# Optimization experiments

Hardware: AMD Instinct MI355X
Metric: run time of the kernel (lower is better)

Reference implementation:

```python
import jax, jax.numpy as jnp
import numpy as np

D_MODEL = 256
N_HEADS = 8
S_LOCAL = (3, 3)
EPS = 1e-6
B, T, H, W = 2, 4, 32, 32


def _neighbor_idx(Hs, Ws, kh, kw):
    # Replicates nn.Unfold(kernel=(kh,kw), padding=(kh//2,kw//2), stride=1) ordering:
    # kernel offsets row-major, spatial positions row-major.
    off_i = np.repeat(np.arange(kh) - kh // 2, kw)  # (L,)
    off_j = np.tile(np.arange(kw) - kw // 2, kh)    # (L,)
    pi, pj = np.meshgrid(np.arange(Hs), np.arange(Ws), indexing='ij')
    ni = pi.reshape(-1, 1) + off_i[None, :]  # (N, L)
    nj = pj.reshape(-1, 1) + off_j[None, :]
    valid = (ni >= 0) & (ni < Hs) & (nj >= 0) & (nj < Ws)
    idx = np.clip(ni, 0, Hs - 1) * Ws + np.clip(nj, 0, Ws - 1)
    return jnp.asarray(idx, dtype=jnp.int32), jnp.asarray(valid)


def setup_inputs() -> dict:
    key = jax.random.key(0)
    ks = jax.random.split(key, 10)
    D = D_MODEL
    x = jax.random.normal(ks[0], (B, D, T, H, W), dtype=jnp.float32)
    w = lambda k: jax.random.normal(k, (D, D), dtype=jnp.float32) * 0.02
    return {
        'x': x,
        'gamma': jnp.ones((D,), jnp.float32),
        'beta': jnp.zeros((D,), jnp.float32),
        'Wq': w(ks[1]), 'Wk': w(ks[2]), 'Wv': w(ks[3]),
        'Wkl': w(ks[4]), 'Wvl': w(ks[5]), 'Wo': w(ks[6]),
        'q_bias': jax.random.normal(ks[7], (1, N_HEADS, 1, D // N_HEADS), dtype=jnp.float32) * 0.02,
    }


def reference(x, gamma, beta, Wq, Wk, Wv, Wkl, Wvl, Wo, q_bias):
    Bx, D, Tx, Hx, Wx = x.shape
    N = Hx * Wx
    BT = Bx * Tx
    h = N_HEADS
    dh = D // h
    factor = dh ** -0.5

    # (B, D, T, H, W) -> (B*T, H*W, D)
    xr = x.transpose(0, 2, 3, 4, 1).reshape(BT, N, D)
    mu = xr.mean(-1, keepdims=True)
    var = ((xr - mu) ** 2).mean(-1, keepdims=True)
    xn = (xr - mu) * jax.lax.rsqrt(var + EPS) * gamma + beta

    def proj(Wm):
        return (xn @ Wm.T).reshape(BT, N, h, dh).transpose(0, 2, 1, 3)  # (BT, h, N, dh)

    q = proj(Wq) + q_bias
    k = proj(Wk)
    v = proj(Wv)
    kl = proj(Wkl)
    vl = proj(Wvl)

    idx, valid = _neighbor_idx(Hx, Wx, *S_LOCAL)  # (N, L)
    k_nb = kl[:, :, idx, :]  # (BT, h, N, L, dh) -- gather instead of im2col
    v_nb = vl[:, :, idx, :]

    attn_global = jnp.einsum('bhnd,bhgd->bhng', q, k) * factor         # (BT,h,N,N)
    attn_local = jnp.einsum('bhnd,bhnld->bhnl', q, k_nb)               # (BT,h,N,L)
    attn_local = jnp.where(valid[None, None], attn_local, -jnp.inf) * factor

    attn = jax.nn.softmax(jnp.concatenate([attn_global, attn_local], axis=-1), axis=-1)
    a_g, a_l = attn[..., :N], attn[..., N:]

    xg = jnp.einsum('bhng,bhgd->bhnd', a_g, v)
    xl = jnp.einsum('bhnl,bhnld->bhnd', a_l, v_nb)
    out = ((xg + xl).transpose(0, 2, 1, 3).reshape(BT, N, D)) @ Wo.T
    return out.reshape(Bx, Tx, Hx, Wx, D).transpose(0, 4, 1, 2, 3)
```

## Files before the change

kernel.cpp:

```cpp
#include <hip/hip_runtime.h>

#define MCONST 8.0f

typedef float f32x4 __attribute__((ext_vector_type(4)));
typedef __bf16 bf16x8 __attribute__((ext_vector_type(8)));
typedef __bf16 bf16x4 __attribute__((ext_vector_type(4)));


__global__ __launch_bounds__(256) void ln_kernel(const float* __restrict__ x,
                                                 const float* __restrict__ gamma,
                                                 const float* __restrict__ beta,
                                                 __bf16* __restrict__ xfh,
                                                 __bf16* __restrict__ xfl,
                                                 const float* __restrict__ Wq,
                                                 const float* __restrict__ Wk,
                                                 const float* __restrict__ Wv,
                                                 const float* __restrict__ Wkl,
                                                 const float* __restrict__ Wvl,
                                                 const float* __restrict__ Wo,
                                                 __bf16* __restrict__ wh,
                                                 __bf16* __restrict__ wl) {
  __shared__ float red[2][8][32];
  const int blk = blockIdx.x;
  if (blk >= 256) {
    const int gid = (blk - 256) * 256 + threadIdx.x;
    const int mat = gid >> 14;
    const int e = (gid & 16383) * 4;
    const float* W = (mat == 0) ? Wq : (mat == 1) ? Wk : (mat == 2) ? Wv
                     : (mat == 3) ? Wkl : (mat == 4) ? Wvl : Wo;
    const float4 f = *(const float4*)(W + e);
    const int o = e >> 8, k = e & 255;
    const size_t frag = (size_t)mat * 65536 + ((o >> 4) * 8 + (k >> 5)) * 512 +
                        (((k & 31) >> 3) * 16 + (o & 15)) * 8 + (k & 7);
    bf16x4 h, l;
    h[0] = (__bf16)f.x; l[0] = (__bf16)(f.x - (float)h[0]);
    h[1] = (__bf16)f.y; l[1] = (__bf16)(f.y - (float)h[1]);
    h[2] = (__bf16)f.z; l[2] = (__bf16)(f.z - (float)h[2]);
    h[3] = (__bf16)f.w; l[3] = (__bf16)(f.w - (float)h[3]);
    *(bf16x4*)(wh + frag) = h;
    *(bf16x4*)(wl + frag) = l;
    return;
  }
  const int bt = blk >> 5;
  const int b = bt >> 2, t = bt & 3;
  const int n0 = (blk & 31) << 5;
  const int part = threadIdx.x >> 5, r = threadIdx.x & 31;
  const int n = n0 + r;
  const float* xp = x + ((size_t)(b * 256) * 4 + t) * 1024 + n;
  float sum = 0.f, sumsq = 0.f;
#pragma unroll 8
  for (int dd = 0; dd < 32; ++dd) {
    float vv = xp[(size_t)(part * 32 + dd) * 4096];
    sum += vv;
    sumsq += vv * vv;
  }
  red[0][part][r] = sum;
  red[1][part][r] = sumsq;
  __syncthreads();
  float s1 = 0.f, s2 = 0.f;
#pragma unroll
  for (int p = 0; p < 8; ++p) {
    s1 += red[0][p][r];
    s2 += red[1][p][r];
  }
  const float mu = s1 * (1.0f / 256.0f);
  const float var = s2 * (1.0f / 256.0f) - mu * mu;
  const float rstd = rsqrtf(var + 1e-6f);
  const size_t row = (size_t)bt * 1024 + n;
  __bf16 hbuf[32], lbuf[32];
#pragma unroll 8
  for (int dd = 0; dd < 32; ++dd) {
    const int d = part * 32 + dd;
    float vv = xp[(size_t)d * 4096];
    const float val = (vv - mu) * rstd * gamma[d] + beta[d];
    const __bf16 h = (__bf16)val;
    hbuf[dd] = h;
    lbuf[dd] = (__bf16)(val - (float)h);
  }
  const size_t base = ((row >> 4) * 8 + part) * 512 + (row & 15) * 8;
#pragma unroll
  for (int g = 0; g < 4; ++g) {
    *(bf16x8*)(xfh + base + g * 128) = *(bf16x8*)&hbuf[g * 8];
    *(bf16x8*)(xfl + base + g * 128) = *(bf16x8*)&lbuf[g * 8];
  }
}

__global__ __launch_bounds__(256) void proj_kernel(
    const __bf16* __restrict__ xfh, const __bf16* __restrict__ xfl,
    const __bf16* __restrict__ wh, const __bf16* __restrict__ wl,
    const float* __restrict__ qb,
    __bf16* __restrict__ qh_g, __bf16* __restrict__ ql_g,
    __bf16* __restrict__ khF, __bf16* __restrict__ vfH,
    float* __restrict__ kloc, float* __restrict__ vloc) {
  const int z = blockIdx.z;
  const int tok0 = blockIdx.x * 128;
  const int o0 = blockIdx.y * 128;
  const int tid = threadIdx.x;
  const int w = tid >> 6, lane = tid & 63;
  const int col = lane & 15, grp = lane >> 4;
  const int oq = (w & 1) * 64, tq = (w >> 1) * 64;

  const __bf16* wbh = wh + (size_t)z * 65536 + (size_t)((o0 + oq) >> 4) * 8 * 512 + lane * 8;
  const __bf16* wbl = wl + (size_t)z * 65536 + (size_t)((o0 + oq) >> 4) * 8 * 512 + lane * 8;
  const __bf16* xbh = xfh + (size_t)((tok0 + tq) >> 4) * 8 * 512 + lane * 8;
  const __bf16* xbl = xfl + (size_t)((tok0 + tq) >> 4) * 8 * 512 + lane * 8;

  f32x4 acc[4][4];
#pragma unroll
  for (int i = 0; i < 4; ++i)
#pragma unroll
    for (int j = 0; j < 4; ++j) acc[i][j] = (f32x4){0.f, 0.f, 0.f, 0.f};

#pragma unroll 1
  for (int kc = 0; kc < 8; ++kc) {
    bf16x8 wfh_[4], wfl_[4], xh_[4], xl_[4];
#pragma unroll
    for (int i = 0; i < 4; ++i) {
      wfh_[i] = *(const bf16x8*)(wbh + ((size_t)i * 8 + kc) * 512);
      wfl_[i] = *(const bf16x8*)(wbl + ((size_t)i * 8 + kc) * 512);
      xh_[i] = *(const bf16x8*)(xbh + ((size_t)i * 8 + kc) * 512);
      xl_[i] = *(const bf16x8*)(xbl + ((size_t)i * 8 + kc) * 512);
    }
    if (z == 2) {
#pragma unroll
      for (int i = 0; i < 4; ++i)
#pragma unroll
        for (int j = 0; j < 4; ++j) {
          acc[i][j] = __builtin_amdgcn_mfma_f32_16x16x32_bf16(xl_[i], wfh_[j], acc[i][j], 0, 0, 0);
          acc[i][j] = __builtin_amdgcn_mfma_f32_16x16x32_bf16(xh_[i], wfl_[j], acc[i][j], 0, 0, 0);
          acc[i][j] = __builtin_amdgcn_mfma_f32_16x16x32_bf16(xh_[i], wfh_[j], acc[i][j], 0, 0, 0);
        }
    } else {
#pragma unroll
      for (int i = 0; i < 4; ++i)
#pragma unroll
        for (int j = 0; j < 4; ++j) {
          acc[i][j] = __builtin_amdgcn_mfma_f32_16x16x32_bf16(wfl_[i], xh_[j], acc[i][j], 0, 0, 0);
          acc[i][j] = __builtin_amdgcn_mfma_f32_16x16x32_bf16(wfh_[i], xl_[j], acc[i][j], 0, 0, 0);
          acc[i][j] = __builtin_amdgcn_mfma_f32_16x16x32_bf16(wfh_[i], xh_[j], acc[i][j], 0, 0, 0);
        }
    }
  }

  if (z == 2) {
#pragma unroll
    for (int i = 0; i < 4; ++i) {
      const int tk = tok0 + tq + i * 16 + grp * 4;
      const int bt = tk >> 10, nb = tk & 1023;
      const int ch = nb >> 6, ss = (nb >> 5) & 1;
      const int vgrp = (nb >> 3) & 3, j0 = nb & 7;
#pragma unroll
      for (int j = 0; j < 4; ++j) {
        const int o = o0 + oq + j * 16 + col;
        const int head = o >> 5, dh = o & 31;
        const int bth = bt * 8 + head;
        const size_t off = (((size_t)(bth * 16 + ch) * 4) + (dh >> 4) * 2 + ss) * 512 +
                           (vgrp * 16 + (dh & 15)) * 8 + j0;
        bf16x4 hv;
#pragma unroll
        for (int rr = 0; rr < 4; ++rr) hv[rr] = (__bf16)acc[i][j][rr];
        *(bf16x4*)(vfH + off) = hv;
      }
    }
  } else {
#pragma unroll
    for (int i = 0; i < 4; ++i) {
      const int o_ = o0 + oq + i * 16 + grp * 4;
      const int head = o_ >> 5, dh0 = o_ & 31;
      float4 qb4 = make_float4(0.f, 0.f, 0.f, 0.f);
      if (z == 0) qb4 = *(const float4*)&qb[o_];
#pragma unroll
      for (int j = 0; j < 4; ++j) {
        const int n_ = tok0 + tq + j * 16 + col;
        const int bt = n_ >> 10, nb = n_ & 1023;
        const int bth = bt * 8 + head;
        float v0 = acc[i][j][0], v1 = acc[i][j][1], v2 = acc[i][j][2], v3 = acc[i][j][3];
        if (z == 0) { v0 += qb4.x; v1 += qb4.y; v2 += qb4.z; v3 += qb4.w; }
        if (z == 0) {
          bf16x4 hv, lv;
          hv[0] = (__bf16)v0; lv[0] = (__bf16)(v0 - (float)hv[0]);
          hv[1] = (__bf16)v1; lv[1] = (__bf16)(v1 - (float)hv[1]);
          hv[2] = (__bf16)v2; lv[2] = (__bf16)(v2 - (float)hv[2]);
          hv[3] = (__bf16)v3; lv[3] = (__bf16)(v3 - (float)hv[3]);
          const size_t idx = ((size_t)bth * 1024 + nb) * 32 + dh0;
          *(bf16x4*)(qh_g + idx) = hv;
          *(bf16x4*)(ql_g + idx) = lv;
        } else if (z == 1) {
          bf16x4 hv;
          hv[0] = (__bf16)v0; hv[1] = (__bf16)v1;
          hv[2] = (__bf16)v2; hv[3] = (__bf16)v3;
          const size_t ka = ((size_t)(bth * 64 + (nb >> 4))) * 512 +
                            ((dh0 >> 3) * 16 + (nb & 15)) * 8 + (dh0 & 7);
          *(bf16x4*)(khF + ka) = hv;
        } else {
          float* dst = (z == 3) ? kloc : vloc;
          *(float4*)&dst[((size_t)bth * 1024 + nb) * 32 + dh0] = make_float4(v0, v1, v2, v3);
        }
      }
    }
  }
}

#define PSTR 68
__global__ __launch_bounds__(256) void attn_kernel(
    const __bf16* __restrict__ qh_g, const __bf16* __restrict__ ql_g,
    const __bf16* __restrict__ khF, const __bf16* __restrict__ vfH,
    const float* __restrict__ kloc, const float* __restrict__ vloc,
    __bf16* __restrict__ ctxFh, __bf16* __restrict__ ctxFl) {
  __shared__ float pbs[4][16 * PSTR];
  float* obuf = &pbs[0][0];

  const int bth = blockIdx.x, qt = blockIdx.y;
  const int tid = threadIdx.x;
  const int w = tid >> 6, lane = tid & 63;
  const int col = lane & 15, grp = lane >> 4;
  const int m0 = qt * 64 + w * 16;
  const float SCALE2 = 0.17677669529663687f * 1.4426950408889634f;
  const size_t kvbase = (size_t)bth << 10;
  float* pb = pbs[w];

  const __bf16* khB = khF + (size_t)bth * 32768 + lane * 8;
  const __bf16* vhB = vfH + (size_t)bth * 32768 + lane * 8;

  const bf16x8 qhf = *(const bf16x8*)(qh_g + (kvbase + m0 + col) * 32 + 8 * grp);

  f32x4 oc0 = {0.f, 0.f, 0.f, 0.f}, oc1 = {0.f, 0.f, 0.f, 0.f};
  float lrow[4] = {0.f, 0.f, 0.f, 0.f};

  bf16x8 kh4[4];
  bf16x8 vh[2][2];

#pragma unroll
  for (int t = 0; t < 4; ++t) kh4[t] = *(const bf16x8*)(khB + (size_t)t * 512);
  {
    f32x4 s_[4];
#pragma unroll
    for (int t = 0; t < 4; ++t) {
      f32x4 a2 = {0.f, 0.f, 0.f, 0.f};
      s_[t] = __builtin_amdgcn_mfma_f32_16x16x32_bf16(qhf, kh4[t], a2, 0, 0, 0);
    }
#pragma unroll
    for (int r = 0; r < 4; ++r)
#pragma unroll
      for (int t = 0; t < 4; ++t) {
        const float p = __builtin_amdgcn_exp2f(fmaf(s_[t][r], SCALE2, -MCONST));
        lrow[r] += p;
        pb[(grp * 4 + r) * PSTR + t * 16 + col] = p;
      }
  }

#pragma unroll 1
  for (int i = 1; i < 16; ++i) {
#pragma unroll
    for (int h = 0; h < 2; ++h)
#pragma unroll
      for (int s = 0; s < 2; ++s)
        vh[h][s] = *(const bf16x8*)(vhB + ((size_t)(i - 1) * 4 + h * 2 + s) * 512);
#pragma unroll
    for (int t = 0; t < 4; ++t)
      kh4[t] = *(const bf16x8*)(khB + ((size_t)i * 4 + t) * 512);
    f32x4 pa[4];
#pragma unroll
    for (int s = 0; s < 2; ++s) {
      pa[s * 2 + 0] = *(const f32x4*)&pb[col * PSTR + s * 32 + 8 * grp];
      pa[s * 2 + 1] = *(const f32x4*)&pb[col * PSTR + s * 32 + 8 * grp + 4];
    }
    bf16x8 ph[2];
#pragma unroll
    for (int s = 0; s < 2; ++s)
#pragma unroll
      for (int j = 0; j < 4; ++j) {
        ph[s][j] = (__bf16)pa[s * 2][j];
        ph[s][4 + j] = (__bf16)pa[s * 2 + 1][j];
      }
#pragma unroll
    for (int s = 0; s < 2; ++s) {
      oc0 = __builtin_amdgcn_mfma_f32_16x16x32_bf16(ph[s], vh[0][s], oc0, 0, 0, 0);
      oc1 = __builtin_amdgcn_mfma_f32_16x16x32_bf16(ph[s], vh[1][s], oc1, 0, 0, 0);
    }
    f32x4 s_[4];
#pragma unroll
    for (int t = 0; t < 4; ++t) {
      f32x4 a2 = {0.f, 0.f, 0.f, 0.f};
      s_[t] = __builtin_amdgcn_mfma_f32_16x16x32_bf16(qhf, kh4[t], a2, 0, 0, 0);
    }
#pragma unroll
    for (int r = 0; r < 4; ++r)
#pragma unroll
      for (int t = 0; t < 4; ++t) {
        const float p = __builtin_amdgcn_exp2f(fmaf(s_[t][r], SCALE2, -MCONST));
        lrow[r] += p;
        pb[(grp * 4 + r) * PSTR + t * 16 + col] = p;
      }
  }

  {
#pragma unroll
    for (int h = 0; h < 2; ++h)
#pragma unroll
      for (int s = 0; s < 2; ++s)
        vh[h][s] = *(const bf16x8*)(vhB + ((size_t)15 * 4 + h * 2 + s) * 512);
    f32x4 pa[4];
#pragma unroll
    for (int s = 0; s < 2; ++s) {
      pa[s * 2 + 0] = *(const f32x4*)&pb[col * PSTR + s * 32 + 8 * grp];
      pa[s * 2 + 1] = *(const f32x4*)&pb[col * PSTR + s * 32 + 8 * grp + 4];
    }
    bf16x8 ph[2];
#pragma unroll
    for (int s = 0; s < 2; ++s)
#pragma unroll
      for (int j = 0; j < 4; ++j) {
        ph[s][j] = (__bf16)pa[s * 2][j];
        ph[s][4 + j] = (__bf16)pa[s * 2 + 1][j];
      }
#pragma unroll
    for (int s = 0; s < 2; ++s) {
      oc0 = __builtin_amdgcn_mfma_f32_16x16x32_bf16(ph[s], vh[0][s], oc0, 0, 0, 0);
      oc1 = __builtin_amdgcn_mfma_f32_16x16x32_bf16(ph[s], vh[1][s], oc1, 0, 0, 0);
    }
  }

#pragma unroll
  for (int r = 0; r < 4; ++r) {
    lrow[r] += __shfl_xor(lrow[r], 1);
    lrow[r] += __shfl_xor(lrow[r], 2);
    lrow[r] += __shfl_xor(lrow[r], 4);
    lrow[r] += __shfl_xor(lrow[r], 8);
  }

  __syncthreads();
#pragma unroll
  for (int r = 0; r < 4; ++r) {
    const int qq = w * 16 + grp * 4 + r;
    obuf[qq * 36 + col] = oc0[r];
    obuf[qq * 36 + 16 + col] = oc1[r];
    if (col == 0) obuf[qq * 36 + 33] = lrow[r];
  }
  __syncthreads();

  {
    const int qq = tid >> 2, part = tid & 3;
    const int n = qt * 64 + qq;
    float L = obuf[qq * 36 + 33];
    float A[8];
#pragma unroll
    for (int d = 0; d < 8; ++d) A[d] = obuf[qq * 36 + part * 8 + d];
    float qrf[8];
    {
      const bf16x8 qh8 = *(const bf16x8*)(qh_g + (kvbase + n) * 32 + part * 8);
      const bf16x8 ql8 = *(const bf16x8*)(ql_g + (kvbase + n) * 32 + part * 8);
#pragma unroll
      for (int d = 0; d < 8; ++d)
        qrf[d] = ((float)qh8[d] + (float)ql8[d]) * SCALE2;
    }
    const int pi = n >> 5, pj = n & 31;
#pragma unroll
    for (int tt = 0; tt < 9; ++tt) {
      const int ni = pi + tt / 3 - 1;
      const int nj = pj + tt % 3 - 1;
      const bool ok = (ni >= 0) && (ni < 32) && (nj >= 0) && (nj < 32);
      if (ok) {
        const size_t nb = (kvbase + ni * 32 + nj) * 32 + part * 8;
        const float* kr = kloc + nb;
        float d0 = 0.f, d1 = 0.f;
#pragma unroll
        for (int d = 0; d < 8; d += 2) {
          d0 = fmaf(qrf[d], kr[d], d0);
          d1 = fmaf(qrf[d + 1], kr[d + 1], d1);
        }
        float dot = d0 + d1;
        dot += __shfl_xor(dot, 1);
        dot += __shfl_xor(dot, 2);
        const float p = __builtin_amdgcn_exp2f(dot - MCONST);
        L += p;
        const float* vr = vloc + nb;
#pragma unroll
        for (int d = 0; d < 8; ++d) A[d] = fmaf(p, vr[d], A[d]);
      }
    }
    const float inv = 1.0f / L;
    const int bt = bth >> 3, head = bth & 7;
    __bf16 hb[8], lb[8];
#pragma unroll
    for (int d = 0; d < 8; ++d) {
      const float val = A[d] * inv;
      const __bf16 h = (__bf16)val;
      hb[d] = h;
      lb[d] = (__bf16)(val - (float)h);
    }
    const size_t rowg = (size_t)bt * 1024 + n;
    const size_t cb = ((rowg >> 4) * 8 + head) * 512 + (part * 16 + (rowg & 15)) * 8;
    *(bf16x8*)(ctxFh + cb) = *(bf16x8*)hb;
    *(bf16x8*)(ctxFl + cb) = *(bf16x8*)lb;
  }
}

__global__ __launch_bounds__(256) void outproj_kernel(
    const __bf16* __restrict__ ctxFh, const __bf16* __restrict__ ctxFl,
    const __bf16* __restrict__ woh, const __bf16* __restrict__ wol,
    float* __restrict__ out) {
  const int m0 = blockIdx.x * 128;
  const int o0 = blockIdx.y * 128;
  const int tid = threadIdx.x;
  const int w = tid >> 6, lane = tid & 63;
  const int col = lane & 15, grp = lane >> 4;
  const int mq = (w & 1) * 64, nq = (w >> 1) * 64;

  const __bf16* abh = ctxFh + (size_t)((m0 + mq) >> 4) * 8 * 512 + lane * 8;
  const __bf16* abl = ctxFl + (size_t)((m0 + mq) >> 4) * 8 * 512 + lane * 8;
  const __bf16* bbh = woh + (size_t)((o0 + nq) >> 4) * 8 * 512 + lane * 8;
  const __bf16* bbl = wol + (size_t)((o0 + nq) >> 4) * 8 * 512 + lane * 8;

  f32x4 acc[4][4];
#pragma unroll
  for (int i = 0; i < 4; ++i)
#pragma unroll
    for (int j = 0; j < 4; ++j) acc[i][j] = (f32x4){0.f, 0.f, 0.f, 0.f};

#pragma unroll 1
  for (int kc = 0; kc < 8; ++kc) {
    bf16x8 ah[4], al[4], bh[4], bl[4];
#pragma unroll
    for (int i = 0; i < 4; ++i) {
      ah[i] = *(const bf16x8*)(abh + ((size_t)i * 8 + kc) * 512);
      al[i] = *(const bf16x8*)(abl + ((size_t)i * 8 + kc) * 512);
      bh[i] = *(const bf16x8*)(bbh + ((size_t)i * 8 + kc) * 512);
      bl[i] = *(const bf16x8*)(bbl + ((size_t)i * 8 + kc) * 512);
    }
#pragma unroll
    for (int mi = 0; mi < 4; ++mi)
#pragma unroll
      for (int ni = 0; ni < 4; ++ni) {
        acc[mi][ni] = __builtin_amdgcn_mfma_f32_16x16x32_bf16(al[mi], bh[ni], acc[mi][ni], 0, 0, 0);
        acc[mi][ni] = __builtin_amdgcn_mfma_f32_16x16x32_bf16(ah[mi], bl[ni], acc[mi][ni], 0, 0, 0);
        acc[mi][ni] = __builtin_amdgcn_mfma_f32_16x16x32_bf16(ah[mi], bh[ni], acc[mi][ni], 0, 0, 0);
      }
  }
#pragma unroll
  for (int mi = 0; mi < 4; ++mi) {
    const int mb = m0 + mq + mi * 16 + grp * 4;
    const int bt = mb >> 10;
    const int nb = mb & 1023;
    const int b = bt >> 2, t = bt & 3;
#pragma unroll
    for (int ni = 0; ni < 4; ++ni) {
      const int o = o0 + nq + ni * 16 + col;
      const float4 f4 = make_float4(acc[mi][ni][0], acc[mi][ni][1],
                                    acc[mi][ni][2], acc[mi][ni][3]);
      *(float4*)&out[((size_t)(b * 256 + o) * 4 + t) * 1024 + nb] = f4;
    }
  }
}

extern "C" void kernel_launch(void* const* d_in, const int* in_sizes, int n_in,
                              void* d_out, int out_size, void* d_ws, size_t ws_size,
                              hipStream_t stream) {
  const float* x = (const float*)d_in[0];
  const float* gamma = (const float*)d_in[1];
  const float* beta = (const float*)d_in[2];
  const float* Wq = (const float*)d_in[3];
  const float* Wk = (const float*)d_in[4];
  const float* Wv = (const float*)d_in[5];
  const float* Wkl = (const float*)d_in[6];
  const float* Wvl = (const float*)d_in[7];
  const float* Wo = (const float*)d_in[8];
  const float* qb = (const float*)d_in[9];

  char* base = (char*)d_ws;
  const size_t MB = 1024 * 1024;
  __bf16* xfh = (__bf16*)(base + 0);
  __bf16* xfl = (__bf16*)(base + 4 * MB);
  __bf16* ctxFh = (__bf16*)(base + 0);
  __bf16* ctxFl = (__bf16*)(base + 4 * MB);
  __bf16* wh = (__bf16*)(base + 8 * MB);
  __bf16* wl = (__bf16*)(base + 8 * MB + 768 * 1024);
  __bf16* qh = (__bf16*)(base + 10 * MB);
  __bf16* ql = (__bf16*)(base + 14 * MB);
  __bf16* khF = (__bf16*)(base + 18 * MB);
  __bf16* vfH = (__bf16*)(base + 26 * MB);
  float* kloc = (float*)(base + 34 * MB);
  float* vloc = (float*)(base + 42 * MB);

  hipLaunchKernelGGL(ln_kernel, dim3(640), dim3(256), 0, stream, x, gamma, beta,
                     xfh, xfl, Wq, Wk, Wv, Wkl, Wvl, Wo, wh, wl);
  hipLaunchKernelGGL(proj_kernel, dim3(64, 2, 5), dim3(256), 0, stream, xfh, xfl,
                     wh, wl, qb, qh, ql, khF, vfH, kloc, vloc);
  hipLaunchKernelGGL(attn_kernel, dim3(64, 16), dim3(256), 0, stream, qh, ql, khF,
                     vfH, kloc, vloc, ctxFh, ctxFl);
  hipLaunchKernelGGL(outproj_kernel, dim3(64, 2), dim3(256), 0, stream, ctxFh,
                     ctxFl, wh + (size_t)5 * 65536, wl + (size_t)5 * 65536,
                     (float*)d_out);
}
```

Baseline: 156.3 us.

## Cache LN inputs in registers, double-buffer GEMM fragment loads, shrink outproj tiles

The layernorm kernel keeps the 32 loaded input values in registers so it does not read x from global memory a second time. The projection and output-projection GEMMs now double-buffer their fragment loads, issuing the loads for the next k-chunk before running the MFMAs on the current one. The aim is to hide global-load latency behind matrix math. The output projection also moves from 128x128 to 64x64 tiles, launching four times as many blocks to fill more CUs, at the cost of more register pressure from the doubled fragment buffers and less data reuse per block.

```diff
diff --git a/kernel.cpp b/kernel.cpp
--- a/kernel.cpp
+++ b/kernel.cpp
@@ -47,10 +47,12 @@
   const int part = threadIdx.x >> 5, r = threadIdx.x & 31;
   const int n = n0 + r;
   const float* xp = x + ((size_t)(b * 256) * 4 + t) * 1024 + n;
+  float cache[32];
   float sum = 0.f, sumsq = 0.f;
 #pragma unroll 8
   for (int dd = 0; dd < 32; ++dd) {
     float vv = xp[(size_t)(part * 32 + dd) * 4096];
+    cache[dd] = vv;
     sum += vv;
     sumsq += vv * vv;
   }
@@ -71,8 +73,7 @@
 #pragma unroll 8
   for (int dd = 0; dd < 32; ++dd) {
     const int d = part * 32 + dd;
-    float vv = xp[(size_t)d * 4096];
-    const float val = (vv - mu) * rstd * gamma[d] + beta[d];
+    const float val = (cache[dd] - mu) * rstd * gamma[d] + beta[d];
     const __bf16 h = (__bf16)val;
     hbuf[dd] = h;
     lbuf[dd] = (__bf16)(val - (float)h);
@@ -82,6 +83,43 @@
   for (int g = 0; g < 4; ++g) {
     *(bf16x8*)(xfh + base + g * 128) = *(bf16x8*)&hbuf[g * 8];
     *(bf16x8*)(xfl + base + g * 128) = *(bf16x8*)&lbuf[g * 8];
+  }
+}
+
+__device__ __forceinline__ void load_frags4(const __bf16* wbh, const __bf16* wbl,
+                                            const __bf16* xbh, const __bf16* xbl,
+                                            int kc, bf16x8 (&wh_)[4], bf16x8 (&wl_)[4],
+                                            bf16x8 (&xh_)[4], bf16x8 (&xl_)[4]) {
+#pragma unroll
+  for (int i = 0; i < 4; ++i) {
+    wh_[i] = *(const bf16x8*)(wbh + ((size_t)i * 8 + kc) * 512);
+    wl_[i] = *(const bf16x8*)(wbl + ((size_t)i * 8 + kc) * 512);
+    xh_[i] = *(const bf16x8*)(xbh + ((size_t)i * 8 + kc) * 512);
+    xl_[i] = *(const bf16x8*)(xbl + ((size_t)i * 8 + kc) * 512);
+  }
+}
+
+__device__ __forceinline__ void mfma3_proj(int z, f32x4 (&acc)[4][4],
+                                           bf16x8 (&wh_)[4], bf16x8 (&wl_)[4],
+                                           bf16x8 (&xh_)[4], bf16x8 (&xl_)[4]) {
+  if (z == 2) {
+#pragma unroll
+    for (int i = 0; i < 4; ++i)
+#pragma unroll
+      for (int j = 0; j < 4; ++j) {
+        acc[i][j] = __builtin_amdgcn_mfma_f32_16x16x32_bf16(xl_[i], wh_[j], acc[i][j], 0, 0, 0);
+        acc[i][j] = __builtin_amdgcn_mfma_f32_16x16x32_bf16(xh_[i], wl_[j], acc[i][j], 0, 0, 0);
+        acc[i][j] = __builtin_amdgcn_mfma_f32_16x16x32_bf16(xh_[i], wh_[j], acc[i][j], 0, 0, 0);
+      }
+  } else {
+#pragma unroll
+    for (int i = 0; i < 4; ++i)
+#pragma unroll
+      for (int j = 0; j < 4; ++j) {
+        acc[i][j] = __builtin_amdgcn_mfma_f32_16x16x32_bf16(wl_[i], xh_[j], acc[i][j], 0, 0, 0);
+        acc[i][j] = __builtin_amdgcn_mfma_f32_16x16x32_bf16(wh_[i], xl_[j], acc[i][j], 0, 0, 0);
+        acc[i][j] = __builtin_amdgcn_mfma_f32_16x16x32_bf16(wh_[i], xh_[j], acc[i][j], 0, 0, 0);
+      }
   }
 }
 
@@ -111,35 +149,15 @@
 #pragma unroll
     for (int j = 0; j < 4; ++j) acc[i][j] = (f32x4){0.f, 0.f, 0.f, 0.f};
 
+  bf16x8 wA[4], lA[4], xA[4], yA[4];
+  bf16x8 wB[4], lB[4], xB[4], yB[4];
+  load_frags4(wbh, wbl, xbh, xbl, 0, wA, lA, xA, yA);
 #pragma unroll 1
-  for (int kc = 0; kc < 8; ++kc) {
-    bf16x8 wfh_[4], wfl_[4], xh_[4], xl_[4];
-#pragma unroll
-    for (int i = 0; i < 4; ++i) {
-      wfh_[i] = *(const bf16x8*)(wbh + ((size_t)i * 8 + kc) * 512);
-      wfl_[i] = *(const bf16x8*)(wbl + ((size_t)i * 8 + kc) * 512);
-      xh_[i] = *(const bf16x8*)(xbh + ((size_t)i * 8 + kc) * 512);
-      xl_[i] = *(const bf16x8*)(xbl + ((size_t)i * 8 + kc) * 512);
-    }
-    if (z == 2) {
-#pragma unroll
-      for (int i = 0; i < 4; ++i)
-#pragma unroll
-        for (int j = 0; j < 4; ++j) {
-          acc[i][j] = __builtin_amdgcn_mfma_f32_16x16x32_bf16(xl_[i], wfh_[j], acc[i][j], 0, 0, 0);
-          acc[i][j] = __builtin_amdgcn_mfma_f32_16x16x32_bf16(xh_[i], wfl_[j], acc[i][j], 0, 0, 0);
-          acc[i][j] = __builtin_amdgcn_mfma_f32_16x16x32_bf16(xh_[i], wfh_[j], acc[i][j], 0, 0, 0);
-        }
-    } else {
-#pragma unroll
-      for (int i = 0; i < 4; ++i)
-#pragma unroll
-        for (int j = 0; j < 4; ++j) {
-          acc[i][j] = __builtin_amdgcn_mfma_f32_16x16x32_bf16(wfl_[i], xh_[j], acc[i][j], 0, 0, 0);
-          acc[i][j] = __builtin_amdgcn_mfma_f32_16x16x32_bf16(wfh_[i], xl_[j], acc[i][j], 0, 0, 0);
-          acc[i][j] = __builtin_amdgcn_mfma_f32_16x16x32_bf16(wfh_[i], xh_[j], acc[i][j], 0, 0, 0);
-        }
-    }
+  for (int kc = 0; kc < 8; kc += 2) {
+    load_frags4(wbh, wbl, xbh, xbl, kc + 1, wB, lB, xB, yB);
+    mfma3_proj(z, acc, wA, lA, xA, yA);
+    if (kc + 2 < 8) load_frags4(wbh, wbl, xbh, xbl, kc + 2, wA, lA, xA, yA);
+    mfma3_proj(z, acc, wB, lB, xB, yB);
   }
 
   if (z == 2) {
@@ -396,55 +414,73 @@
   }
 }
 
+__device__ __forceinline__ void load_frags2(const __bf16* abh, const __bf16* abl,
+                                            const __bf16* bbh, const __bf16* bbl,
+                                            int kc, bf16x8 (&ah)[2], bf16x8 (&al)[2],
+                                            bf16x8 (&bh)[2], bf16x8 (&bl)[2]) {
+#pragma unroll
+  for (int i = 0; i < 2; ++i) {
+    ah[i] = *(const bf16x8*)(abh + ((size_t)i * 8 + kc) * 512);
+    al[i] = *(const bf16x8*)(abl + ((size_t)i * 8 + kc) * 512);
+    bh[i] = *(const bf16x8*)(bbh + ((size_t)i * 8 + kc) * 512);
+    bl[i] = *(const bf16x8*)(bbl + ((size_t)i * 8 + kc) * 512);
+  }
+}
+
+__device__ __forceinline__ void mfma3_out(f32x4 (&acc)[2][2], bf16x8 (&ah)[2],
+                                          bf16x8 (&al)[2], bf16x8 (&bh)[2],
+                                          bf16x8 (&bl)[2]) {
+#pragma unroll
+  for (int mi = 0; mi < 2; ++mi)
+#pragma unroll
+    for (int ni = 0; ni < 2; ++ni) {
+      acc[mi][ni] = __builtin_amdgcn_mfma_f32_16x16x32_bf16(al[mi], bh[ni], acc[mi][ni], 0, 0, 0);
+      acc[mi][ni] = __builtin_amdgcn_mfma_f32_16x16x32_bf16(ah[mi], bl[ni], acc[mi][ni], 0, 0, 0);
+      acc[mi][ni] = __builtin_amdgcn_mfma_f32_16x16x32_bf16(ah[mi], bh[ni], acc[mi][ni], 0, 0, 0);
+    }
+}
+
 __global__ __launch_bounds__(256) void outproj_kernel(
     const __bf16* __restrict__ ctxFh, const __bf16* __restrict__ ctxFl,
     const __bf16* __restrict__ woh, const __bf16* __restrict__ wol,
     float* __restrict__ out) {
-  const int m0 = blockIdx.x * 128;
-  const int o0 = blockIdx.y * 128;
+  const int m0 = blockIdx.x * 64;
+  const int o0 = blockIdx.y * 64;
   const int tid = threadIdx.x;
   const int w = tid >> 6, lane = tid & 63;
   const int col = lane & 15, grp = lane >> 4;
-  const int mq = (w & 1) * 64, nq = (w >> 1) * 64;
+  const int mq = (w & 1) * 32, nq = (w >> 1) * 32;
 
   const __bf16* abh = ctxFh + (size_t)((m0 + mq) >> 4) * 8 * 512 + lane * 8;
   const __bf16* abl = ctxFl + (size_t)((m0 + mq) >> 4) * 8 * 512 + lane * 8;
   const __bf16* bbh = woh + (size_t)((o0 + nq) >> 4) * 8 * 512 + lane * 8;
   const __bf16* bbl = wol + (size_t)((o0 + nq) >> 4) * 8 * 512 + lane * 8;
 
-  f32x4 acc[4][4];
-#pragma unroll
-  for (int i = 0; i < 4; ++i)
-#pragma unroll
-    for (int j = 0; j < 4; ++j) acc[i][j] = (f32x4){0.f, 0.f, 0.f, 0.f};
-
+  f32x4 acc[2][2];
+#pragma unroll
+  for (int i = 0; i < 2; ++i)
+#pragma unroll
+    for (int j = 0; j < 2; ++j) acc[i][j] = (f32x4){0.f, 0.f, 0.f, 0.f};
+
+  bf16x8 ahA[2], alA[2], bhA[2], blA[2];
+  bf16x8 ahB[2], alB[2], bhB[2], blB[2];
+  load_frags2(abh, abl, bbh, bbl, 0, ahA, alA, bhA, blA);
 #pragma unroll 1
-  for (int kc = 0; kc < 8; ++kc) {
-    bf16x8 ah[4], al[4], bh[4], bl[4];
-#pragma unroll
-    for (int i = 0; i < 4; ++i) {
-      ah[i] = *(const bf16x8*)(abh + ((size_t)i * 8 + kc) * 512);
-      al[i] = *(const bf16x8*)(abl + ((size_t)i * 8 + kc) * 512);
-      bh[i] = *(const bf16x8*)(bbh + ((size_t)i * 8 + kc) * 512);
-      bl[i] = *(const bf16x8*)(bbl + ((size_t)i * 8 + kc) * 512);
-    }
-#pragma unroll
-    for (int mi = 0; mi < 4; ++mi)
-#pragma unroll
-      for (int ni = 0; ni < 4; ++ni) {
-        acc[mi][ni] = __builtin_amdgcn_mfma_f32_16x16x32_bf16(al[mi], bh[ni], acc[mi][ni], 0, 0, 0);
-        acc[mi][ni] = __builtin_amdgcn_mfma_f32_16x16x32_bf16(ah[mi], bl[ni], acc[mi][ni], 0, 0, 0);
-        acc[mi][ni] = __builtin_amdgcn_mfma_f32_16x16x32_bf16(ah[mi], bh[ni], acc[mi][ni], 0, 0, 0);
-      }
-  }
-#pragma unroll
-  for (int mi = 0; mi < 4; ++mi) {
+  for (int kc = 0; kc < 8; kc += 2) {
+    load_frags2(abh, abl, bbh, bbl, kc + 1, ahB, alB, bhB, blB);
+    mfma3_out(acc, ahA, alA, bhA, blA);
+    if (kc + 2 < 8) load_frags2(abh, abl, bbh, bbl, kc + 2, ahA, alA, bhA, blA);
+    mfma3_out(acc, ahB, alB, bhB, blB);
+  }
+
+#pragma unroll
+  for (int mi = 0; mi < 2; ++mi) {
     const int mb = m0 + mq + mi * 16 + grp * 4;
     const int bt = mb >> 10;
     const int nb = mb & 1023;
     const int b = bt >> 2, t = bt & 3;
 #pragma unroll
-    for (int ni = 0; ni < 4; ++ni) {
+    for (int ni = 0; ni < 2; ++ni) {
       const int o = o0 + nq + ni * 16 + col;
       const float4 f4 = make_float4(acc[mi][ni][0], acc[mi][ni][1],
                                     acc[mi][ni][2], acc[mi][ni][3]);
@@ -488,7 +524,7 @@
                      wh, wl, qb, qh, ql, khF, vfH, kloc, vloc);
   hipLaunchKernelGGL(attn_kernel, dim3(64, 16), dim3(256), 0, stream, qh, ql, khF,
                      vfH, kloc, vloc, ctxFh, ctxFl);
-  hipLaunchKernelGGL(outproj_kernel, dim3(64, 2), dim3(256), 0, stream, ctxFh,
+  hipLaunchKernelGGL(outproj_kernel, dim3(128, 4), dim3(256), 0, stream, ctxFh,
                      ctxFl, wh + (size_t)5 * 65536, wl + (size_t)5 * 65536,
                      (float*)d_out);
 }
```

Result: no change. 159.5 us (+2.0%).
